# Optimization experiments

Hardware: AMD Instinct MI355X
Metric: run time of the kernel (lower is better)

Reference implementation:

```python
import jax, jax.numpy as jnp
import numpy as np

K = 20          # neighbors
BN_EPS = 1e-5


def _knn_idx(x, k):
    """x: [B, C, N] -> idx of k nearest neighbors [B, N, k] (by squared distance, self included)."""
    xx = jnp.sum(x * x, axis=1)                       # [B, N]
    inner = jnp.einsum('bcn,bcm->bnm', x, x)          # [B, N, N]
    neg_sqdist = 2.0 * inner - xx[:, :, None] - xx[:, None, :]
    return jax.lax.top_k(neg_sqdist, k)[1]            # [B, N, k]


def _graph_feature(x, k):
    """x: [B, C, N] -> edge features cat(x_j - x_i, x_i): [B, 2C, N, k]."""
    idx = _knn_idx(x, k)                              # [B, N, k]
    xT = x.transpose(0, 2, 1)                         # [B, N, C]
    nbrs = jax.vmap(lambda xt, ii: xt[ii])(xT, idx)   # [B, N, k, C] gather
    center = xT[:, :, None, :]                        # [B, N, 1, C]
    feat = jnp.concatenate(
        [nbrs - center, jnp.broadcast_to(center, nbrs.shape)], axis=-1)  # [B, N, k, 2C]
    return feat.transpose(0, 3, 1, 2)                 # [B, 2C, N, k]


def _conv_bn_lrelu(feat, W, gamma, beta, mean, var):
    """1x1 Conv2d (no bias) + BatchNorm (given stats) + LeakyReLU(0.2). feat: [B, Cin, N, k]."""
    y = jnp.einsum('oc,bcnk->bonk', W, feat)
    scale = (gamma / jnp.sqrt(var + BN_EPS))[None, :, None, None]
    y = (y - mean[None, :, None, None]) * scale + beta[None, :, None, None]
    return jnp.where(y > 0, y, 0.2 * y)


def setup_inputs() -> dict:
    key = jax.random.key(0)
    ks = list(jax.random.split(key, 32))
    B, N = 8, 1024
    f32 = jnp.float32

    def w(kk, o, i):
        return jax.random.normal(kk, (o, i), dtype=f32) / np.sqrt(i)

    def bn(k1, k2, k3, k4, c):
        g = jax.random.uniform(k1, (c,), dtype=f32, minval=0.5, maxval=1.5)
        b = jax.random.normal(k2, (c,), dtype=f32) * 0.05
        m = jax.random.normal(k3, (c,), dtype=f32) * 0.05
        v = jax.random.uniform(k4, (c,), dtype=f32, minval=0.5, maxval=1.5)
        return g, b, m, v

    x = jax.random.normal(ks[0], (B, N, 3), dtype=f32)
    W0 = w(ks[1], 64, 6);    g0, b0, m0, v0 = bn(ks[2], ks[3], ks[4], ks[5], 64)
    W1 = w(ks[6], 128, 128); g1, b1, m1, v1 = bn(ks[7], ks[8], ks[9], ks[10], 128)
    W2 = w(ks[11], 256, 256); g2, b2, m2, v2 = bn(ks[12], ks[13], ks[14], ks[15], 256)
    Wf = w(ks[16], 512, 896); gf, bf, mf, vf = bn(ks[17], ks[18], ks[19], ks[20], 512)
    We = w(ks[21], 256, 512)
    return dict(x=x,
                W0=W0, g0=g0, b0=b0, m0=m0, v0=v0,
                W1=W1, g1=g1, b1=b1, m1=m1, v1=v1,
                W2=W2, g2=g2, b2=b2, m2=m2, v2=v2,
                Wf=Wf, gf=gf, bf=bf, mf=mf, vf=vf,
                We=We)


def reference(x, W0, g0, b0, m0, v0, W1, g1, b1, m1, v1,
              W2, g2, b2, m2, v2, Wf, gf, bf, mf, vf, We):
    h = x.transpose(0, 2, 1)                          # [B, 3, N]
    outs = []
    for (W, g, b, m, v) in ((W0, g0, b0, m0, v0),
                            (W1, g1, b1, m1, v1),
                            (W2, g2, b2, m2, v2)):
        gfeat = _graph_feature(h, K)                  # [B, 2C, N, k]
        y = _conv_bn_lrelu(gfeat, W, g, b, m, v)      # [B, Cout, N, k]
        h = y.mean(axis=-1)                           # max-free EdgeConv pool over k
        outs.append(h)
    cat = jnp.concatenate(outs, axis=1)               # [B, 448, N]
    gfeat = _graph_feature(cat, K)                    # [B, 896, N, k]
    y = _conv_bn_lrelu(gfeat, Wf, gf, bf, mf, vf)     # [B, 512, N, k]
    pooled = y.mean(axis=-1).mean(axis=-1)            # [B, 512] (pool over k then N)
    return pooled @ We.T                              # [B, num_features]
```

## Files before the change

kernel.cpp:

```cpp
#include <hip/hip_runtime.h>
#include <cstdint>

#define KNN 20
#define BV 8
#define NV 1024

template <int CTRL>
__device__ __forceinline__ unsigned dppmax(unsigned x) {
    unsigned m = (unsigned)__builtin_amdgcn_update_dpp((int)x, (int)x, CTRL, 0xf, 0xf, false);
    return (x > m) ? x : m;
}
template <int CTRL>
__device__ __forceinline__ unsigned dppmin(unsigned x) {
    unsigned m = (unsigned)__builtin_amdgcn_update_dpp((int)x, (int)x, CTRL, 0xf, 0xf, false);
    return (x < m) ? x : m;
}
__device__ __forceinline__ unsigned wave_max_u32(unsigned x) {
    x = dppmax<0xB1>(x); x = dppmax<0x4E>(x); x = dppmax<0x141>(x);
    x = dppmax<0x140>(x); x = dppmax<0x142>(x); x = dppmax<0x143>(x);
    return (unsigned)__builtin_amdgcn_readlane((int)x, 63);
}
__device__ __forceinline__ unsigned wave_min_u32(unsigned x) {
    x = dppmin<0xB1>(x); x = dppmin<0x4E>(x); x = dppmin<0x141>(x);
    x = dppmin<0x140>(x); x = dppmin<0x142>(x); x = dppmin<0x143>(x);
    return (unsigned)__builtin_amdgcn_readlane((int)x, 63);
}

__global__ __launch_bounds__(256) void k_transpose(const float* __restrict__ x, float* __restrict__ hx) {
    int id = blockIdx.x * 256 + threadIdx.x;
    if (id >= BV * 3 * NV) return;
    int n = id % NV;
    int c = (id / NV) % 3;
    int b = id / (3 * NV);
    hx[id] = x[(b * NV + n) * 3 + c];
}

__global__ __launch_bounds__(256) void k_xx(const float* __restrict__ h, float* __restrict__ xx,
                                            int C, int bstride) {
    int id = blockIdx.x * 256 + threadIdx.x;
    int n = id % NV, b = id / NV;
    if (b >= BV) return;
    const float* hp = h + (size_t)b * bstride + n;
    float s = 0.f;
    for (int c = 0; c < C; ++c) { float v = hp[(size_t)c * NV]; s += v * v; }
    xx[b * NV + n] = s;
}

__global__ __launch_bounds__(256, 4) void k_knn(const float* __restrict__ h, const float* __restrict__ xx,
                                                int C, int bstride, int* __restrict__ idx) {
    __shared__ float Bs[8][1024];
    const int b = blockIdx.y, i0 = blockIdx.x * 8;
    const int t = threadIdx.x, lane = t & 63, w = t >> 6;
    const int irow = i0 + w * 2;
    float acc[2][16] = {};
    const float* hb = h + (size_t)b * bstride;

    for (int c0 = 0; c0 < C; c0 += 8) {
        __syncthreads();
#pragma unroll
        for (int r = 0; r < 8; ++r) {
            int e = r * 256 + t;
            int cc = e >> 8, jj = e & 255;
            float4 v = make_float4(0.f, 0.f, 0.f, 0.f);
            if (c0 + cc < C) v = *(const float4*)&hb[(size_t)(c0 + cc) * NV + jj * 4];
            *(float4*)&Bs[cc][jj * 4] = v;
        }
        __syncthreads();
#pragma unroll
        for (int c = 0; c < 8; ++c) {
            float2 arv = *(const float2*)&Bs[c][irow];
            float ar[2] = {arv.x, arv.y};
            float br[16];
#pragma unroll
            for (int g = 0; g < 4; ++g) {
                float4 bv = *(const float4*)&Bs[c][g * 256 + (lane << 2)];
                br[g * 4 + 0] = bv.x; br[g * 4 + 1] = bv.y;
                br[g * 4 + 2] = bv.z; br[g * 4 + 3] = bv.w;
            }
#pragma unroll
            for (int a = 0; a < 2; ++a)
#pragma unroll
                for (int q = 0; q < 16; ++q) acc[a][q] += ar[a] * br[q];
        }
    }

    const float* xb = xx + b * NV;
    float xxj[16];
#pragma unroll
    for (int g = 0; g < 4; ++g) {
        float4 xv = *(const float4*)&xb[g * 256 + (lane << 2)];
        xxj[g * 4 + 0] = xv.x; xxj[g * 4 + 1] = xv.y;
        xxj[g * 4 + 2] = xv.z; xxj[g * 4 + 3] = xv.w;
    }
#pragma unroll
    for (int a = 0; a < 2; ++a) {
        float xi = xb[irow + a];
#pragma unroll
        for (int q = 0; q < 16; ++q) acc[a][q] = 2.f * acc[a][q] - xi - xxj[q];
    }

    int* opb = idx + ((size_t)(b * NV + irow)) * KNN;
#pragma unroll 1
    for (int s = 0; s < KNN; ++s) {
#pragma unroll
        for (int a = 0; a < 2; ++a) {
            float v0[8]; int q0[8];
#pragma unroll
            for (int i = 0; i < 8; ++i) {
                bool g = acc[a][2 * i + 1] > acc[a][2 * i];
                v0[i] = g ? acc[a][2 * i + 1] : acc[a][2 * i];
                q0[i] = g ? 2 * i + 1 : 2 * i;
            }
            float v1[4]; int q1[4];
#pragma unroll
            for (int i = 0; i < 4; ++i) {
                bool g = v0[2 * i + 1] > v0[2 * i];
                v1[i] = g ? v0[2 * i + 1] : v0[2 * i];
                q1[i] = g ? q0[2 * i + 1] : q0[2 * i];
            }
            float v2[2]; int q2[2];
#pragma unroll
            for (int i = 0; i < 2; ++i) {
                bool g = v1[2 * i + 1] > v1[2 * i];
                v2[i] = g ? v1[2 * i + 1] : v1[2 * i];
                q2[i] = g ? q1[2 * i + 1] : q1[2 * i];
            }
            bool gf = v2[1] > v2[0];
            float bv = gf ? v2[1] : v2[0];
            int bq = gf ? q2[1] : q2[0];

            unsigned u = __float_as_uint(bv);
            unsigned su = ((int)u < 0) ? ~u : (u | 0x80000000u);
            int myj = ((bq >> 2) << 8) | (lane << 2) | (bq & 3);
            unsigned gmax = wave_max_u32(su);
            unsigned cand = (su == gmax) ? (unsigned)myj : 0xFFFFFFFFu;
            int j = (int)wave_min_u32(cand);
            if (lane == 0) opb[a * KNN + s] = j;
            int wq = (myj == j && su == gmax) ? bq : 99;
#pragma unroll
            for (int q = 0; q < 16; ++q)
                if (wq == q) acc[a][q] = -3.4e38f;
        }
    }
}

__global__ __launch_bounds__(256) void k_pack(const float* __restrict__ W, float* __restrict__ wb,
                                              int C, int O) {
    int id = blockIdx.x * 256 + threadIdx.x;
    if (id >= 2 * O * C) return;
    int c = id % C, o = (id / C) % O, half = id / (C * O);
    float wl = W[(size_t)o * 2 * C + c];
    wb[id] = half ? (W[(size_t)o * 2 * C + C + c] - wl) : wl;
}

__global__ __launch_bounds__(256) void k_gemm(const float* __restrict__ A, int astride,
                                              const float* __restrict__ h, int bstride, int C,
                                              float* __restrict__ out, int O) {
    __shared__ float Ws[8][64], Hs[8][128];
    const int b = blockIdx.z, o0 = blockIdx.y * 64, n0 = blockIdx.x * 128;
    const int t = threadIdx.x, tx = t & 15, ty = t >> 4;
    float acc[4][8] = {};
    const float* hb = h + (size_t)b * bstride;
    for (int c0 = 0; c0 < C; c0 += 8) {
#pragma unroll
        for (int q = 0; q < 2; ++q) {
            int e = t + q * 256;
            int oo = e >> 3, cc = e & 7;
            Ws[cc][oo] = ((c0 + cc) < C) ? A[(size_t)(o0 + oo) * astride + c0 + cc] : 0.f;
        }
        {
            int cc = t >> 5, nn4 = t & 31;
            float4 v = make_float4(0.f, 0.f, 0.f, 0.f);
            if (c0 + cc < C) v = *(const float4*)&hb[(size_t)(c0 + cc) * NV + n0 + nn4 * 4];
            *(float4*)&Hs[cc][nn4 * 4] = v;
        }
        __syncthreads();
#pragma unroll
        for (int c = 0; c < 8; ++c) {
            float4 wv = *(const float4*)&Ws[c][ty * 4];
            float ar[4] = {wv.x, wv.y, wv.z, wv.w};
            float br[8];
            float4 h0 = *(const float4*)&Hs[c][tx * 4];
            float4 h1 = *(const float4*)&Hs[c][64 + tx * 4];
            br[0] = h0.x; br[1] = h0.y; br[2] = h0.z; br[3] = h0.w;
            br[4] = h1.x; br[5] = h1.y; br[6] = h1.z; br[7] = h1.w;
#pragma unroll
            for (int a = 0; a < 4; ++a)
#pragma unroll
                for (int q = 0; q < 8; ++q) acc[a][q] += ar[a] * br[q];
        }
        __syncthreads();
    }
#pragma unroll
    for (int a = 0; a < 4; ++a) {
        int o = o0 + ty * 4 + a;
        float* outp = out + ((size_t)b * O + o) * NV + n0;
        float4 s0 = make_float4(acc[a][0], acc[a][1], acc[a][2], acc[a][3]);
        float4 s1 = make_float4(acc[a][4], acc[a][5], acc[a][6], acc[a][7]);
        *(float4*)&outp[tx * 4] = s0;
        *(float4*)&outp[64 + tx * 4] = s1;
    }
}

__global__ __launch_bounds__(256) void k_edge(const float* __restrict__ pd,
                                              const int* __restrict__ idx,
                                              const float* __restrict__ ga, const float* __restrict__ be,
                                              const float* __restrict__ mu, const float* __restrict__ va,
                                              float* __restrict__ out, int out_bstride, int O) {
    const int n = blockIdx.x * 256 + threadIdx.x;
    const int o = blockIdx.y, b = blockIdx.z;
    const float a  = ga[o] / sqrtf(va[o] + 1e-5f);
    const float c0 = be[o] - mu[o] * a;
    const float* pb = pd + ((size_t)b * 2 * O + o) * NV;
    const float dv  = pd[((size_t)b * 2 * O + O + o) * NV + n];
    const int* ip   = idx + ((size_t)b * NV + n) * KNN;
    float s = 0.f;
#pragma unroll
    for (int k = 0; k < KNN; ++k) {
        int j = ip[k];
        float y = fmaf(a, pb[j] + dv, c0);
        s += (y > 0.f) ? y : 0.2f * y;
    }
    out[(size_t)b * out_bstride + (size_t)o * NV + n] = s * (1.f / KNN);
}

__global__ __launch_bounds__(256) void k_pool(const float* __restrict__ hf, float* __restrict__ pooled) {
    const int o = blockIdx.x, b = blockIdx.y;
    const float* hp = hf + ((size_t)b * 512 + o) * NV;
    float s = 0.f;
    for (int i = threadIdx.x; i < NV; i += 256) s += hp[i];
#pragma unroll
    for (int off = 32; off > 0; off >>= 1) s += __shfl_down(s, off, 64);
    __shared__ float red[4];
    if ((threadIdx.x & 63) == 0) red[threadIdx.x >> 6] = s;
    __syncthreads();
    if (threadIdx.x == 0)
        pooled[(size_t)b * 512 + o] = (red[0] + red[1] + red[2] + red[3]) * (1.f / NV);
}

__global__ __launch_bounds__(256) void k_final(const float* __restrict__ pooled, const float* __restrict__ We,
                                               float* __restrict__ out) {
    const int j = threadIdx.x, b = blockIdx.x;
    __shared__ float ps[512];
    for (int o = threadIdx.x; o < 512; o += 256) ps[o] = pooled[b * 512 + o];
    __syncthreads();
    float s = 0.f;
    for (int o = 0; o < 512; ++o) s += ps[o] * We[(size_t)j * 512 + o];
    out[b * 256 + j] = s;
}

extern "C" void kernel_launch(void* const* d_in, const int* in_sizes, int n_in,
                              void* d_out, int out_size, void* d_ws, size_t ws_size,
                              hipStream_t stream) {
    const float* x  = (const float*)d_in[0];
    const float* W0 = (const float*)d_in[1];
    const float* g0 = (const float*)d_in[2];
    const float* b0 = (const float*)d_in[3];
    const float* m0 = (const float*)d_in[4];
    const float* v0 = (const float*)d_in[5];
    const float* W1 = (const float*)d_in[6];
    const float* g1 = (const float*)d_in[7];
    const float* b1 = (const float*)d_in[8];
    const float* m1 = (const float*)d_in[9];
    const float* v1 = (const float*)d_in[10];
    const float* W2 = (const float*)d_in[11];
    const float* g2 = (const float*)d_in[12];
    const float* b2 = (const float*)d_in[13];
    const float* m2 = (const float*)d_in[14];
    const float* v2 = (const float*)d_in[15];
    const float* Wf = (const float*)d_in[16];
    const float* gf = (const float*)d_in[17];
    const float* bf = (const float*)d_in[18];
    const float* mf = (const float*)d_in[19];
    const float* vf = (const float*)d_in[20];
    const float* We = (const float*)d_in[21];

    float* ws = (float*)d_ws;
    float* hx     = ws;
    float* cat    = hx + 24576;
    float* xx     = cat + 3670016;
    int*   idx    = (int*)(xx + 8192);
    float* pd     = (float*)(idx + 163840);
    float* wb     = pd + 8388608;
    float* hf     = wb + 458752;
    float* pooled = hf + 4194304;

    k_transpose<<<96, 256, 0, stream>>>(x, hx);

    auto run_layer = [&](const float* h, int C, int bstride, const float* W,
                         const float* g, const float* be, const float* m, const float* v,
                         int O, float* outp, int obstride) {
        k_xx<<<32, 256, 0, stream>>>(h, xx, C, bstride);
        k_knn<<<dim3(128, 8), 256, 0, stream>>>(h, xx, C, bstride, idx);
        int pn = 2 * O * C;
        k_pack<<<(pn + 255) / 256, 256, 0, stream>>>(W, wb, C, O);
        k_gemm<<<dim3(8, 2 * O / 64, 8), 256, 0, stream>>>(wb, C, h, bstride, C, pd, 2 * O);
        k_edge<<<dim3(4, O, 8), 256, 0, stream>>>(pd, idx, g, be, m, v, outp, obstride, O);
    };

    run_layer(hx, 3, 3 * NV, W0, g0, b0, m0, v0, 64, cat, 448 * NV);
    run_layer(cat, 64, 448 * NV, W1, g1, b1, m1, v1, 128, cat + 64 * NV, 448 * NV);
    run_layer(cat + 64 * NV, 128, 448 * NV, W2, g2, b2, m2, v2, 256, cat + 192 * NV, 448 * NV);
    run_layer(cat, 448, 448 * NV, Wf, gf, bf, mf, vf, 512, hf, 512 * NV);

    k_pool<<<dim3(512, 8), 256, 0, stream>>>(hf, pooled);
    k_final<<<8, 256, 0, stream>>>(pooled, We, (float*)d_out);
}
```

Measured before the change: 887.1 us.

## Widen kNN blocks, select on sortable uints, reorder grids, batch channels in edge

The kNN kernel moves to 512-thread blocks covering 16 query rows, flattening the batch into the block index. Distances are converted once to order-preserving unsigned keys so the per-step argmax tree works on integers and drops the per-step float-to-uint conversion. The gemm and edge grids are reordered to put batch first, and the edge kernel now loads the neighbor indices once and reuses them across four output channels. Larger kNN blocks can lower occupancy, and the edge kernel's gathers now touch several channel rows per thread.

```diff
diff --git a/kernel.cpp b/kernel.cpp
--- a/kernel.cpp
+++ b/kernel.cpp
@@ -46,10 +46,12 @@
     xx[b * NV + n] = s;
 }
 
-__global__ __launch_bounds__(256, 4) void k_knn(const float* __restrict__ h, const float* __restrict__ xx,
+__global__ __launch_bounds__(512, 4) void k_knn(const float* __restrict__ h, const float* __restrict__ xx,
                                                 int C, int bstride, int* __restrict__ idx) {
     __shared__ float Bs[8][1024];
-    const int b = blockIdx.y, i0 = blockIdx.x * 8;
+    const int bx = blockIdx.x;
+    const int b = bx & 7, tile = bx >> 3;
+    const int i0 = tile * 16;
     const int t = threadIdx.x, lane = t & 63, w = t >> 6;
     const int irow = i0 + w * 2;
     float acc[2][16] = {};
@@ -58,8 +60,8 @@
     for (int c0 = 0; c0 < C; c0 += 8) {
         __syncthreads();
 #pragma unroll
-        for (int r = 0; r < 8; ++r) {
-            int e = r * 256 + t;
+        for (int r = 0; r < 4; ++r) {
+            int e = r * 512 + t;
             int cc = e >> 8, jj = e & 255;
             float4 v = make_float4(0.f, 0.f, 0.f, 0.f);
             if (c0 + cc < C) v = *(const float4*)&hb[(size_t)(c0 + cc) * NV + jj * 4];
@@ -92,11 +94,16 @@
         xxj[g * 4 + 0] = xv.x; xxj[g * 4 + 1] = xv.y;
         xxj[g * 4 + 2] = xv.z; xxj[g * 4 + 3] = xv.w;
     }
+    unsigned ua[2][16];
 #pragma unroll
     for (int a = 0; a < 2; ++a) {
         float xi = xb[irow + a];
 #pragma unroll
-        for (int q = 0; q < 16; ++q) acc[a][q] = 2.f * acc[a][q] - xi - xxj[q];
+        for (int q = 0; q < 16; ++q) {
+            float d = 2.f * acc[a][q] - xi - xxj[q];
+            unsigned u = __float_as_uint(d);
+            ua[a][q] = ((int)u < 0) ? ~u : (u | 0x80000000u);
+        }
     }
 
     int* opb = idx + ((size_t)(b * NV + irow)) * KNN;
@@ -104,42 +111,41 @@
     for (int s = 0; s < KNN; ++s) {
 #pragma unroll
         for (int a = 0; a < 2; ++a) {
-            float v0[8]; int q0[8];
+            unsigned w0[8]; int p0[8];
 #pragma unroll
             for (int i = 0; i < 8; ++i) {
-                bool g = acc[a][2 * i + 1] > acc[a][2 * i];
-                v0[i] = g ? acc[a][2 * i + 1] : acc[a][2 * i];
-                q0[i] = g ? 2 * i + 1 : 2 * i;
+                bool g = ua[a][2 * i + 1] > ua[a][2 * i];
+                w0[i] = g ? ua[a][2 * i + 1] : ua[a][2 * i];
+                p0[i] = g ? 2 * i + 1 : 2 * i;
             }
-            float v1[4]; int q1[4];
+            unsigned w1[4]; int p1[4];
 #pragma unroll
             for (int i = 0; i < 4; ++i) {
-                bool g = v0[2 * i + 1] > v0[2 * i];
-                v1[i] = g ? v0[2 * i + 1] : v0[2 * i];
-                q1[i] = g ? q0[2 * i + 1] : q0[2 * i];
+                bool g = w1[0], gg = w0[2 * i + 1] > w0[2 * i];
+                (void)g;
+                w1[i] = gg ? w0[2 * i + 1] : w0[2 * i];
+                p1[i] = gg ? p0[2 * i + 1] : p0[2 * i];
             }
-            float v2[2]; int q2[2];
+            unsigned w2[2]; int p2[2];
 #pragma unroll
             for (int i = 0; i < 2; ++i) {
-                bool g = v1[2 * i + 1] > v1[2 * i];
-                v2[i] = g ? v1[2 * i + 1] : v1[2 * i];
-                q2[i] = g ? q1[2 * i + 1] : q1[2 * i];
+                bool gg = w1[2 * i + 1] > w1[2 * i];
+                w2[i] = gg ? w1[2 * i + 1] : w1[2 * i];
+                p2[i] = gg ? p1[2 * i + 1] : p1[2 * i];
             }
-            bool gf = v2[1] > v2[0];
-            float bv = gf ? v2[1] : v2[0];
-            int bq = gf ? q2[1] : q2[0];
-
-            unsigned u = __float_as_uint(bv);
-            unsigned su = ((int)u < 0) ? ~u : (u | 0x80000000u);
-            int myj = ((bq >> 2) << 8) | (lane << 2) | (bq & 3);
+            bool gf = w2[1] > w2[0];
+            unsigned su = gf ? w2[1] : w2[0];
+            int bq = gf ? p2[1] : p2[0];
+
             unsigned gmax = wave_max_u32(su);
+            int myj = ((bq >> 2) << 8) + (lane << 2) + (bq & 3);
             unsigned cand = (su == gmax) ? (unsigned)myj : 0xFFFFFFFFu;
             int j = (int)wave_min_u32(cand);
             if (lane == 0) opb[a * KNN + s] = j;
-            int wq = (myj == j && su == gmax) ? bq : 99;
+            int wq = (cand == (unsigned)j) ? bq : 99;
 #pragma unroll
             for (int q = 0; q < 16; ++q)
-                if (wq == q) acc[a][q] = -3.4e38f;
+                if (wq == q) ua[a][q] = 0u;
         }
     }
 }
@@ -157,7 +163,7 @@
                                               const float* __restrict__ h, int bstride, int C,
                                               float* __restrict__ out, int O) {
     __shared__ float Ws[8][64], Hs[8][128];
-    const int b = blockIdx.z, o0 = blockIdx.y * 64, n0 = blockIdx.x * 128;
+    const int b = blockIdx.x, n0 = blockIdx.y * 128, o0 = blockIdx.z * 64;
     const int t = threadIdx.x, tx = t & 15, ty = t >> 4;
     float acc[4][8] = {};
     const float* hb = h + (size_t)b * bstride;
@@ -207,21 +213,28 @@
                                               const float* __restrict__ ga, const float* __restrict__ be,
                                               const float* __restrict__ mu, const float* __restrict__ va,
                                               float* __restrict__ out, int out_bstride, int O) {
-    const int n = blockIdx.x * 256 + threadIdx.x;
-    const int o = blockIdx.y, b = blockIdx.z;
-    const float a  = ga[o] / sqrtf(va[o] + 1e-5f);
-    const float c0 = be[o] - mu[o] * a;
-    const float* pb = pd + ((size_t)b * 2 * O + o) * NV;
-    const float dv  = pd[((size_t)b * 2 * O + O + o) * NV + n];
-    const int* ip   = idx + ((size_t)b * NV + n) * KNN;
-    float s = 0.f;
-#pragma unroll
-    for (int k = 0; k < KNN; ++k) {
-        int j = ip[k];
-        float y = fmaf(a, pb[j] + dv, c0);
-        s += (y > 0.f) ? y : 0.2f * y;
-    }
-    out[(size_t)b * out_bstride + (size_t)o * NV + n] = s * (1.f / KNN);
+    const int b = blockIdx.x;
+    const int n = blockIdx.y * 256 + threadIdx.x;
+    const int o0 = blockIdx.z * 4;
+    const int* ip = idx + ((size_t)b * NV + n) * KNN;
+    int jj[KNN];
+#pragma unroll
+    for (int k = 0; k < KNN; ++k) jj[k] = ip[k];
+#pragma unroll
+    for (int a = 0; a < 4; ++a) {
+        const int o = o0 + a;
+        const float al = ga[o] / sqrtf(va[o] + 1e-5f);
+        const float c0 = be[o] - mu[o] * al;
+        const float* pb = pd + ((size_t)b * 2 * O + o) * NV;
+        const float dv  = pd[((size_t)b * 2 * O + O + o) * NV + n];
+        float s = 0.f;
+#pragma unroll
+        for (int k = 0; k < KNN; ++k) {
+            float y = fmaf(al, pb[jj[k]] + dv, c0);
+            s += (y > 0.f) ? y : 0.2f * y;
+        }
+        out[(size_t)b * out_bstride + (size_t)o * NV + n] = s * (1.f / KNN);
+    }
 }
 
 __global__ __launch_bounds__(256) void k_pool(const float* __restrict__ hf, float* __restrict__ pooled) {
@@ -291,11 +304,11 @@
                          const float* g, const float* be, const float* m, const float* v,
                          int O, float* outp, int obstride) {
         k_xx<<<32, 256, 0, stream>>>(h, xx, C, bstride);
-        k_knn<<<dim3(128, 8), 256, 0, stream>>>(h, xx, C, bstride, idx);
+        k_knn<<<512, 512, 0, stream>>>(h, xx, C, bstride, idx);
         int pn = 2 * O * C;
         k_pack<<<(pn + 255) / 256, 256, 0, stream>>>(W, wb, C, O);
-        k_gemm<<<dim3(8, 2 * O / 64, 8), 256, 0, stream>>>(wb, C, h, bstride, C, pd, 2 * O);
-        k_edge<<<dim3(4, O, 8), 256, 0, stream>>>(pd, idx, g, be, m, v, outp, obstride, O);
+        k_gemm<<<dim3(8, 8, 2 * O / 64), 256, 0, stream>>>(wb, C, h, bstride, C, pd, 2 * O);
+        k_edge<<<dim3(8, 4, O / 4), 256, 0, stream>>>(pd, idx, g, be, m, v, outp, obstride, O);
     };
 
     run_layer(hx, 3, 3 * NV, W0, g0, b0, m0, v0, 64, cat, 448 * NV);
```

Result: faster. 802.6 us (-9.5%).
